# Kernel optimization log

Measured on AMD Instinct MI355X. Metric: run time of the kernel, lower is better.

The kernel has to match this reference:

```python
import jax, jax.numpy as jnp
import numpy as np

N, E, H, IN_NF, G, STEPS, EHID = 4096, 8192, 128, 64, 8, 3, 32


def setup_inputs() -> dict:
    key = jax.random.key(0)
    ks = jax.random.split(key, 24)

    def gn(k, shape, fan_in):
        return jax.random.normal(k, shape, dtype=jnp.float32) / np.sqrt(fan_in)

    inp = {
        "x": jax.random.normal(ks[0], (N, IN_NF), dtype=jnp.float32),
        "edge_index": jax.random.randint(ks[1], (2, E), 0, N, dtype=jnp.int32),
        "edge_attr": jax.random.uniform(ks[2], (E, 1), dtype=jnp.float32),
        "batch": jnp.sort(jax.random.randint(ks[3], (N,), 0, G, dtype=jnp.int32)),
        # lin0: in_nf -> hid
        "lin0_w": gn(ks[4], (IN_NF, H), IN_NF),
        "lin0_b": jnp.zeros((H,), jnp.float32),
        # per-step edge MLP: 1 -> 32 -> H*H (stacked over STEPS)
        "nn_w1": gn(ks[5], (STEPS, 1, EHID), 1),
        "nn_b1": jnp.zeros((STEPS, EHID), jnp.float32),
        "nn_w2": gn(ks[6], (STEPS, EHID, H * H), EHID) * 0.1,
        "nn_b2": jnp.zeros((STEPS, H * H), jnp.float32),
        # NNConv root weight (no bias) + conv bias, per step
        "root_w": gn(ks[7], (STEPS, H, H), H),
        "conv_b": jnp.zeros((STEPS, H), jnp.float32),
        # single-layer GRU (input H, hidden H); gate order r, z, n
        "gru_wih": gn(ks[8], (3 * H, H), H),
        "gru_whh": gn(ks[9], (3 * H, H), H),
        "gru_bih": jnp.zeros((3 * H,), jnp.float32),
        "gru_bhh": jnp.zeros((3 * H,), jnp.float32),
        # readout
        "lin1_w": gn(ks[10], (H, H // 2), H),
        "lin1_b": jnp.zeros((H // 2,), jnp.float32),
        "lin2_w": gn(ks[11], (H // 2, 1), H // 2),
        "lin2_b": jnp.zeros((1,), jnp.float32),
    }
    return inp


def _gru_cell(m, h, wih, whh, bih, bhh):
    gi = m @ wih.T + bih          # [N, 3H]
    gh = h @ whh.T + bhh          # [N, 3H]
    i_r, i_z, i_n = jnp.split(gi, 3, axis=-1)
    h_r, h_z, h_n = jnp.split(gh, 3, axis=-1)
    r = jax.nn.sigmoid(i_r + h_r)
    z = jax.nn.sigmoid(i_z + h_z)
    n = jnp.tanh(i_n + r * h_n)
    return (1.0 - z) * n + z * h


def reference(x, edge_index, edge_attr, batch, lin0_w, lin0_b, nn_w1, nn_b1,
              nn_w2, nn_b2, root_w, conv_b, gru_wih, gru_whh, gru_bih,
              gru_bhh, lin1_w, lin1_b, lin2_w, lin2_b):
    n_nodes = x.shape[0]
    row, col = edge_index[0], edge_index[1]  # source j -> target i

    x = jax.nn.relu(x @ lin0_w + lin0_b)     # [N, H]
    h = x

    # in-degree for mean aggregation (0-degree nodes -> 0 output)
    deg = jax.ops.segment_sum(jnp.ones((row.shape[0],), x.dtype), col,
                              num_segments=n_nodes)
    inv_deg = jnp.where(deg > 0, 1.0 / jnp.maximum(deg, 1.0), 0.0)[:, None]

    for t in range(STEPS):
        # edge-conditioned weights: [E, H, H]
        e_h = jax.nn.relu(edge_attr @ nn_w1[t] + nn_b1[t])
        w_e = (e_h @ nn_w2[t] + nn_b2[t]).reshape(-1, H, H)
        # gather -> per-edge matvec -> scatter-mean
        msg = jnp.einsum('eh,eho->eo', x[row], w_e)
        agg = jax.ops.segment_sum(msg, col, num_segments=n_nodes) * inv_deg
        m = jax.nn.relu(agg + x @ root_w[t] + conv_b[t])
        h = _gru_cell(m, h, gru_wih, gru_whh, gru_bih, gru_bhh)
        x = h

    # global mean pool over graphs
    cnt = jax.ops.segment_sum(jnp.ones((n_nodes,), x.dtype), batch,
                              num_segments=G)
    g = jax.ops.segment_sum(x, batch, num_segments=G) / jnp.maximum(cnt, 1.0)[:, None]
    g = jax.nn.relu(g @ lin1_w + lin1_b)  # dropout: eval mode (identity)
    out = g @ lin2_w + lin2_b             # [G, 1]
    return out
```

## Files before the change

### kernel.cpp

```cpp
#include <hip/hip_runtime.h>
#include <math.h>

#define NN 4096
#define EE 8192
#define HH 128
#define GG 8
#define MU 4096

typedef __attribute__((ext_vector_type(8))) _Float16 half8;
typedef __attribute__((ext_vector_type(4))) float floatx4;

__device__ __forceinline__ void ldst16(const _Float16* g, void* l) {
    __builtin_amdgcn_global_load_lds(
        (const __attribute__((address_space(1))) unsigned int*)g,
        (__attribute__((address_space(3))) unsigned int*)l, 16, 0, 0);
}

__device__ __forceinline__ unsigned f2u(float f) {
    unsigned b = __float_as_uint(f);
    return (b & 0x80000000u) ? ~b : (b | 0x80000000u);
}
__device__ __forceinline__ float u2f(unsigned u) {
    return __uint_as_float((u & 0x80000000u) ? (u ^ 0x80000000u) : ~u);
}

__device__ __forceinline__ int cls_k(float w, float b, float mn, float mx) {
    const float hi = w > 0.f ? w * mx + b : w * mn + b;
    const float lo = w > 0.f ? w * mn + b : w * mx + b;
    if (hi <= 0.f) return 0;
    if (lo >= 0.f) return 1;
    return 2;
}

__global__ __launch_bounds__(256) void ymix_k(
    const _Float16* __restrict__ A, const _Float16* __restrict__ BT3t,
    const float* __restrict__ w2t, _Float16* __restrict__ Y,
    _Float16* __restrict__ U, const int* __restrict__ kflag)
{
    __shared__ __align__(16) _Float16 As[128 * 32];
    __shared__ __align__(16) _Float16 Bs[128 * 32];
    const int tid = threadIdx.x;
    const int lane = tid & 63, wave = tid >> 6;
    const int m0 = blockIdx.y * 128;
    const int wr = (wave >> 1) * 64, wc = (wave & 1) * 64;
    const int fm = lane & 15, fq = lane >> 4;
    const int srow = tid >> 2, soff = (tid & 3) << 3;
    const _Float16* gA0 = A + (size_t)(m0 + srow) * 128 + soff;
    const _Float16* gA1 = gA0 + (size_t)64 * 128;
    char* lA0 = (char*)As + tid * 16;  char* lA1 = (char*)As + (tid + 256) * 16;
    char* lB0 = (char*)Bs + tid * 16;  char* lB1 = (char*)Bs + (tid + 256) * 16;
    const int bx = blockIdx.x;
    const int er = fq * 4, ec = fm;

    floatx4 acc[4][4] = {};
    if (bx < 3) {
        const _Float16* gB0 = BT3t + (size_t)(bx * 128 + srow) * 128 + soff;
        const _Float16* gB1 = gB0 + (size_t)64 * 128;
        for (int k0 = 0; k0 < 128; k0 += 32) {
            __syncthreads();
            ldst16(gA0 + k0, lA0); ldst16(gA1 + k0, lA1);
            ldst16(gB0 + k0, lB0); ldst16(gB1 + k0, lB1);
            __syncthreads();
            half8 af[4], bf[4];
#pragma unroll
            for (int i = 0; i < 4; ++i)
                af[i] = *(const half8*)&As[(wr + i * 16 + fm) * 32 + fq * 8];
#pragma unroll
            for (int j = 0; j < 4; ++j)
                bf[j] = *(const half8*)&Bs[(wc + j * 16 + fm) * 32 + fq * 8];
#pragma unroll
            for (int i = 0; i < 4; ++i)
#pragma unroll
                for (int j = 0; j < 4; ++j)
                    acc[i][j] = __builtin_amdgcn_mfma_f32_16x16x32_f16(
                        af[i], bf[j], acc[i][j], 0, 0, 0);
        }
#pragma unroll
        for (int i = 0; i < 4; ++i) {
            const int gr = m0 + wr + i * 16 + er;
#pragma unroll
            for (int j = 0; j < 4; ++j) {
                const int gc = bx * 128 + wc + j * 16 + ec;
#pragma unroll
                for (int r = 0; r < 4; ++r)
                    Y[(size_t)(gr + r) * 384 + gc] = (_Float16)acc[i][j][r];
            }
        }
    } else {
        const unsigned f = *(const unsigned*)kflag;
        const int kk = bx - 3;
        if (!((f >> kk) & 1u)) return;
        const int cbase = __popc(f & ((1u << kk) - 1u)) << 7;
        const float* w2s = w2t + (size_t)kk * 16384;
        for (int k0 = 0; k0 < 128; k0 += 32) {
            __syncthreads();
            ldst16(gA0 + k0, lA0); ldst16(gA1 + k0, lA1);
#pragma unroll
            for (int c = tid; c < 512; c += 256) {
                const int row = c >> 2, seg = (c & 3) << 3;
                _Float16 v8[8];
#pragma unroll
                for (int u = 0; u < 8; ++u)
                    v8[u] = (_Float16)w2s[(size_t)(k0 + seg + u) * 128 + row];
                *(half8*)&Bs[row * 32 + seg] = *(half8*)v8;
            }
            __syncthreads();
            half8 af[4], bf[4];
#pragma unroll
            for (int i = 0; i < 4; ++i)
                af[i] = *(const half8*)&As[(wr + i * 16 + fm) * 32 + fq * 8];
#pragma unroll
            for (int j = 0; j < 4; ++j)
                bf[j] = *(const half8*)&Bs[(wc + j * 16 + fm) * 32 + fq * 8];
#pragma unroll
            for (int i = 0; i < 4; ++i)
#pragma unroll
                for (int j = 0; j < 4; ++j)
                    acc[i][j] = __builtin_amdgcn_mfma_f32_16x16x32_f16(
                        af[i], bf[j], acc[i][j], 0, 0, 0);
        }
#pragma unroll
        for (int i = 0; i < 4; ++i) {
            const int gr = m0 + wr + i * 16 + er;
#pragma unroll
            for (int j = 0; j < 4; ++j) {
                const int gc = cbase + wc + j * 16 + ec;
#pragma unroll
                for (int r = 0; r < 4; ++r)
                    U[(size_t)(gr + r) * MU + gc] = (_Float16)acc[i][j][r];
            }
        }
    }
}

__global__ __launch_bounds__(256) void escat_k(
    const int2* __restrict__ rc, const float2* __restrict__ ec2,
    const float* __restrict__ ehPt, const _Float16* __restrict__ Y,
    const _Float16* __restrict__ U, float* __restrict__ mpre,
    const int* __restrict__ kflag)
{
    const int b = blockIdx.x;
    const int p0 = ((b & 7) * 512 + (b >> 3)) * 2;
    const int h2 = threadIdx.x >> 7;
    const int o = threadIdx.x & 127;
    const int p = p0 + h2;
    const int2 e = rc[p];
    const float2 c = ec2[p];
    const _Float16* Yr = Y + (size_t)e.x * 384;
    float acc = c.x * (float)Yr[o] + c.y * (float)Yr[128 + o];
    const unsigned f = *(const unsigned*)kflag;
    if (f) {
        const int nk = __popc(f);
        const _Float16* Ur = U + (size_t)e.x * MU;
        const float* ep = ehPt + (size_t)p * 32;
        for (int i = 0; i < nk; ++i)
            acc += ep[i] * (float)Ur[i * 128 + o];
    }
    atomicAdd(&mpre[(size_t)e.y * 128 + o], acc);
}

__global__ __launch_bounds__(256) void gru_k(
    const float* __restrict__ mpre, const _Float16* __restrict__ Y,
    const float* __restrict__ cb, const _Float16* __restrict__ Ax,
    const _Float16* __restrict__ Bih, const _Float16* __restrict__ Bhh,
    const float* __restrict__ bih, const float* __restrict__ bhh,
    float* __restrict__ g1, float* __restrict__ g2)
{
    const int z = blockIdx.z;
    const _Float16* B = z ? Bhh : Bih;
    const float* bias = z ? bhh : bih;
    float* C = z ? g2 : g1;

    __shared__ __align__(16) _Float16 As[128 * 40];
    __shared__ __align__(16) _Float16 Bs[128 * 40];
    const int tid = threadIdx.x;
    const int lane = tid & 63, wave = tid >> 6;
    const int m0 = blockIdx.y * 128, n0 = blockIdx.x * 128;
    const int wr = (wave >> 1) * 64, wc = (wave & 1) * 64;
    const int fm = lane & 15, fq = lane >> 4;

    floatx4 acc[4][4] = {};
    for (int k0 = 0; k0 < 128; k0 += 32) {
        __syncthreads();
#pragma unroll
        for (int c = tid; c < 512; c += 256) {
            const int row = c >> 2, seg = (c & 3) << 3;
            if (z == 0) {
                const int mr = m0 + row;
                const half8 yv = *(const half8*)&Y[(size_t)mr * 384 + 256 + k0 + seg];
                const float4 a0 = *(const float4*)&mpre[(size_t)mr * 128 + k0 + seg];
                const float4 a1 = *(const float4*)&mpre[(size_t)mr * 128 + k0 + seg + 4];
                const float4 c0 = *(const float4*)&cb[k0 + seg];
                const float4 c1 = *(const float4*)&cb[k0 + seg + 4];
                _Float16 v8[8];
                float v;
                v = (float)yv[0] + a0.x + c0.x; v8[0] = (_Float16)(v > 0.f ? v : 0.f);
                v = (float)yv[1] + a0.y + c0.y; v8[1] = (_Float16)(v > 0.f ? v : 0.f);
                v = (float)yv[2] + a0.z + c0.z; v8[2] = (_Float16)(v > 0.f ? v : 0.f);
                v = (float)yv[3] + a0.w + c0.w; v8[3] = (_Float16)(v > 0.f ? v : 0.f);
                v = (float)yv[4] + a1.x + c1.x; v8[4] = (_Float16)(v > 0.f ? v : 0.f);
                v = (float)yv[5] + a1.y + c1.y; v8[5] = (_Float16)(v > 0.f ? v : 0.f);
                v = (float)yv[6] + a1.z + c1.z; v8[6] = (_Float16)(v > 0.f ? v : 0.f);
                v = (float)yv[7] + a1.w + c1.w; v8[7] = (_Float16)(v > 0.f ? v : 0.f);
                *(half8*)&As[row * 40 + seg] = *(half8*)v8;
            } else {
                *(half8*)&As[row * 40 + seg] =
                    *(const half8*)&Ax[(size_t)(m0 + row) * 128 + k0 + seg];
            }
            *(half8*)&Bs[row * 40 + seg] =
                *(const half8*)&B[(size_t)(n0 + row) * 128 + k0 + seg];
        }
        __syncthreads();
        half8 af[4], bf[4];
#pragma unroll
        for (int i = 0; i < 4; ++i)
            af[i] = *(const half8*)&As[(wr + i * 16 + fm) * 40 + fq * 8];
#pragma unroll
        for (int j = 0; j < 4; ++j)
            bf[j] = *(const half8*)&Bs[(wc + j * 16 + fm) * 40 + fq * 8];
#pragma unroll
        for (int i = 0; i < 4; ++i)
#pragma unroll
            for (int j = 0; j < 4; ++j)
                acc[i][j] = __builtin_amdgcn_mfma_f32_16x16x32_f16(
                    af[i], bf[j], acc[i][j], 0, 0, 0);
    }
    const int er = fq * 4, ec = fm;
#pragma unroll
    for (int i = 0; i < 4; ++i) {
        const int gr = m0 + wr + i * 16 + er;
#pragma unroll
        for (int j = 0; j < 4; ++j) {
            const int gc = n0 + wc + j * 16 + ec;
            const float bv = bias[gc];
#pragma unroll
            for (int r = 0; r < 4; ++r)
                C[(size_t)(gr + r) * 384 + gc] = acc[i][j][r] + bv;
        }
    }
}

__global__ void gate_k(const float* __restrict__ G1, const float* __restrict__ G2,
                       float* __restrict__ xh, _Float16* __restrict__ Ax,
                       const int* __restrict__ batch, float* __restrict__ pooled) {
    const int idx = blockIdx.x * 256 + threadIdx.x;
    const int n = idx >> 7, o = idx & 127;
    const size_t b = (size_t)n * 384;
    float ir = G1[b + o], iz = G1[b + 128 + o], in_ = G1[b + 256 + o];
    float hr = G2[b + o], hz = G2[b + 128 + o], hn = G2[b + 256 + o];
    float r = 1.f / (1.f + expf(-(ir + hr)));
    float z = 1.f / (1.f + expf(-(iz + hz)));
    float nv = tanhf(in_ + r * hn);
    float hv = (1.f - z) * nv + z * xh[idx];
    xh[idx] = hv;
    Ax[idx] = (_Float16)hv;
    if (pooled) atomicAdd(&pooled[batch[n] * 128 + o], hv);
}

__global__ __launch_bounds__(256) void setup_lin0_k(
    const float* __restrict__ wih, const float* __restrict__ whh,
    _Float16* __restrict__ Bih, _Float16* __restrict__ Bhh,
    const int* __restrict__ ei, const float* __restrict__ eattr,
    const int* __restrict__ batch,
    float* __restrict__ deg, int* __restrict__ odeg, float* __restrict__ cnt,
    unsigned* __restrict__ eaMM,
    const float* __restrict__ x, const float* __restrict__ l0w,
    const float* __restrict__ l0b, float* __restrict__ xh,
    _Float16* __restrict__ Ax)
{
    __shared__ float loc8[GG];
    __shared__ float As[16][64];
    __shared__ float Bs[16][64];
    const int b = blockIdx.x, t = threadIdx.x;
    if (b < 192) {
        const int idx = b * 256 + t;
        Bih[idx] = (_Float16)wih[idx];
        Bhh[idx] = (_Float16)whh[idx];
    } else if (b < 224) {
        const int e = (b - 192) * 256 + t;
        atomicAdd(&deg[ei[EE + e]], 1.0f);
        atomicAdd(&odeg[ei[e]], 1);
        const float ea = eattr[e];
        unsigned u1 = f2u(ea), u2 = f2u(-ea);
#pragma unroll
        for (int off = 32; off > 0; off >>= 1) {
            unsigned o1 = __shfl_down(u1, off), o2 = __shfl_down(u2, off);
            u1 = u1 > o1 ? u1 : o1;  u2 = u2 > o2 ? u2 : o2;
        }
        if ((t & 63) == 0) { atomicMax(&eaMM[0], u1); atomicMax(&eaMM[1], u2); }
    } else if (b < 240) {
        const int n = (b - 224) * 256 + t;
        if (t < GG) loc8[t] = 0.f;
        __syncthreads();
        atomicAdd(&loc8[batch[n]], 1.0f);
        __syncthreads();
        if (t < GG) atomicAdd(&cnt[t], loc8[t]);
    } else {
        const int bb = b - 240;
        const int j0 = (bb & 1) * 64;
        const int m0 = (bb >> 1) * 64;
        const int tx = t & 15, ty = t >> 4;
        const int arow = t >> 2, acol = (t & 3) << 2;
        const int bk = t >> 4, bj = (t & 15) << 2;
        float c[4][4] = {};
        for (int k0 = 0; k0 < 64; k0 += 16) {
            __syncthreads();
            float4 av = *(const float4*)&x[(size_t)(m0 + arow) * 64 + k0 + acol];
            As[acol + 0][arow] = av.x;
            As[acol + 1][arow] = av.y;
            As[acol + 2][arow] = av.z;
            As[acol + 3][arow] = av.w;
            *(float4*)&Bs[bk][bj] = *(const float4*)&l0w[(size_t)(k0 + bk) * 128 + j0 + bj];
            __syncthreads();
#pragma unroll
            for (int kk = 0; kk < 16; ++kk) {
                const float4 a = *(const float4*)&As[kk][ty << 2];
                const float4 bv = *(const float4*)&Bs[kk][tx << 2];
                c[0][0] += a.x * bv.x; c[0][1] += a.x * bv.y; c[0][2] += a.x * bv.z; c[0][3] += a.x * bv.w;
                c[1][0] += a.y * bv.x; c[1][1] += a.y * bv.y; c[1][2] += a.y * bv.z; c[1][3] += a.y * bv.w;
                c[2][0] += a.z * bv.x; c[2][1] += a.z * bv.y; c[2][2] += a.z * bv.z; c[2][3] += a.z * bv.w;
                c[3][0] += a.w * bv.x; c[3][1] += a.w * bv.y; c[3][2] += a.w * bv.z; c[3][3] += a.w * bv.w;
            }
        }
        const float4 bv = *(const float4*)&l0b[j0 + (tx << 2)];
        const int col0 = j0 + (tx << 2);
#pragma unroll
        for (int i = 0; i < 4; ++i) {
            const int row = m0 + (ty << 2) + i;
            float4 o;
            o.x = fmaxf(c[i][0] + bv.x, 0.f); o.y = fmaxf(c[i][1] + bv.y, 0.f);
            o.z = fmaxf(c[i][2] + bv.z, 0.f); o.w = fmaxf(c[i][3] + bv.w, 0.f);
            *(float4*)&xh[(size_t)row * 128 + col0] = o;
            _Float16* base = Ax + (size_t)row * 128 + col0;
            base[0] = (_Float16)o.x; base[1] = (_Float16)o.y;
            base[2] = (_Float16)o.z; base[3] = (_Float16)o.w;
        }
    }
}

__global__ __launch_bounds__(256) void scan_wsum_k(
    const int* __restrict__ odeg, int* __restrict__ ocur,
    const float* __restrict__ w1, const float* __restrict__ b1,
    const float* __restrict__ w2, const float* __restrict__ b2,
    const float* __restrict__ rw, const unsigned* __restrict__ eaMM,
    _Float16* __restrict__ BT3)
{
    const int t = threadIdx.x;
    if (blockIdx.x == 0) {
        __shared__ int ps[256];
        const int base = t * 16;
        int l[16]; int s = 0;
#pragma unroll
        for (int i = 0; i < 16; ++i) { l[i] = s; s += odeg[base + i]; }
        ps[t] = s;
        __syncthreads();
        for (int d = 1; d < 256; d <<= 1) {
            int v = (t >= d) ? ps[t - d] : 0;
            __syncthreads();
            ps[t] += v;
            __syncthreads();
        }
        const int excl = (t == 0) ? 0 : ps[t - 1];
#pragma unroll
        for (int i = 0; i < 16; ++i) ocur[base + i] = excl + l[i];
    } else {
        __shared__ float wl[32], bl[32];
        const int bb = blockIdx.x - 1;
        const int st = bb >> 6;
        if (t < 32) {
            const float w = w1[st * 32 + t], bv = b1[st * 32 + t];
            const float mx = u2f(eaMM[0]), mn = -u2f(eaMM[1]);
            const int c = cls_k(w, bv, mn, mx);
            wl[t] = (c == 1) ? w : 0.f;
            bl[t] = (c == 1) ? bv : 0.f;
        }
        __syncthreads();
        const int idx = (bb & 63) * 256 + t;
        const int h = idx >> 7, o = idx & 127;
        const float* W2t = w2 + (size_t)st * 524288;
        float a = 0.f, c2 = 0.f;
#pragma unroll 8
        for (int j = 0; j < 32; ++j) {
            const float v = W2t[(size_t)j * 16384 + idx];
            a += wl[j] * v; c2 += bl[j] * v;
        }
        c2 += b2[(size_t)st * 16384 + idx];
        _Float16* B = BT3 + (size_t)st * 49152;
        B[(size_t)o * 128 + h]         = (_Float16)a;
        B[(size_t)(128 + o) * 128 + h] = (_Float16)c2;
        B[(size_t)(256 + o) * 128 + h] = (_Float16)rw[(size_t)st * 16384 + idx];
    }
}

__global__ __launch_bounds__(256) void scatter_k(
    const int* __restrict__ ei, const float* __restrict__ eattr,
    const float* __restrict__ w1, const float* __restrict__ b1,
    const float* __restrict__ deg, int* __restrict__ ocur,
    const unsigned* __restrict__ eaMM,
    int2* __restrict__ rc, float2* __restrict__ ec2,
    float* __restrict__ ehP, int* __restrict__ kflag)
{
    __shared__ unsigned mm[3];
    if (threadIdx.x < 3) mm[threadIdx.x] = 0u;
    __syncthreads();
    if (threadIdx.x < 96) {
        const int tt = threadIdx.x >> 5, k = threadIdx.x & 31;
        const float w = w1[tt * 32 + k], bv = b1[tt * 32 + k];
        const float mx = u2f(eaMM[0]), mn = -u2f(eaMM[1]);
        if (cls_k(w, bv, mn, mx) == 2) atomicOr(&mm[tt], 1u << k);
    }
    __syncthreads();
    const int wave = threadIdx.x >> 6, lane = threadIdx.x & 63;
    const int e = blockIdx.x * 4 + wave;
    const int r = ei[e], c = ei[EE + e];
    int pos = 0;
    if (lane == 0) pos = atomicAdd(&ocur[r], 1);
    pos = __shfl(pos, 0);
    const float d = deg[c];
    const float inv = d > 0.f ? 1.0f / d : 0.0f;
    const float ea = eattr[e];
    if (lane == 0) {
        rc[pos] = make_int2(r, c);
        ec2[pos] = make_float2(ea * inv, inv);
    }
#pragma unroll
    for (int t = 0; t < 3; ++t) {
        const unsigned m = mm[t];
        if (lane < 32 && ((m >> lane) & 1u)) {
            const float v = ea * w1[t * 32 + lane] + b1[t * 32 + lane];
            const int slot = __popc(m & ((1u << lane) - 1u));
            ehP[((size_t)t * EE + pos) * 32 + slot] = (v > 0.f ? v : 0.f) * inv;
        }
    }
    if (threadIdx.x < 3) kflag[threadIdx.x] = (int)mm[threadIdx.x];
}

__global__ __launch_bounds__(128) void final_k(
    const float* __restrict__ pooled, const float* __restrict__ cnt,
    const float* __restrict__ l1w, const float* __restrict__ l1b,
    const float* __restrict__ l2w, const float* __restrict__ l2b,
    float* __restrict__ out)
{
    __shared__ float gv[128];
    const int g = blockIdx.x, t = threadIdx.x;
    float c = cnt[g]; c = c > 1.f ? c : 1.f;
    gv[t] = pooled[g * 128 + t] / c;
    __syncthreads();
    if (t < 64) {
        float y = l1b[t];
        for (int h = 0; h < 128; ++h) y += gv[h] * l1w[h * 64 + t];
        y = y > 0.f ? y : 0.f;
        float s = y * l2w[t];
#pragma unroll
        for (int off = 32; off > 0; off >>= 1)
            s += __shfl_down(s, off);
        if (t == 0) out[g] = s + l2b[0];
    }
}

extern "C" void kernel_launch(void* const* d_in, const int* in_sizes, int n_in,
                              void* d_out, int out_size, void* d_ws, size_t ws_size,
                              hipStream_t stream) {
    const float* x      = (const float*)d_in[0];
    const int*   ei     = (const int*)d_in[1];
    const float* eattr  = (const float*)d_in[2];
    const int*   batch  = (const int*)d_in[3];
    const float* lin0_w = (const float*)d_in[4];
    const float* lin0_b = (const float*)d_in[5];
    const float* nn_w1  = (const float*)d_in[6];
    const float* nn_b1  = (const float*)d_in[7];
    const float* nn_w2  = (const float*)d_in[8];
    const float* nn_b2  = (const float*)d_in[9];
    const float* root_w = (const float*)d_in[10];
    const float* conv_b = (const float*)d_in[11];
    const float* gwih   = (const float*)d_in[12];
    const float* gwhh   = (const float*)d_in[13];
    const float* gbih   = (const float*)d_in[14];
    const float* gbhh   = (const float*)d_in[15];
    const float* l1w    = (const float*)d_in[16];
    const float* l1b    = (const float*)d_in[17];
    const float* l2w    = (const float*)d_in[18];
    const float* l2b    = (const float*)d_in[19];
    float* out = (float*)d_out;
    float* ws  = (float*)d_ws;

    float*    mpre0  = ws;
    float*    pooled = ws + 1572864;
    float*    cnt    = ws + 1573888;
    float*    deg    = ws + 1573896;
    int*      odeg   = (int*)(ws + 1577992);
    unsigned* eaMM   = (unsigned*)(ws + 1582088);
    int*      kflag  = (int*)(ws + 1582090);
    int*      ocur   = (int*)(ws + 1582096);
    int2*     rc     = (int2*)(ws + 1586192);
    float2*   ec2    = (float2*)(ws + 1602576);
    float*    ehP    = ws + 1618960;
    float*    xh     = ws + 2405392;
    float*    g1     = ws + 2929680;
    float*    g2     = ws + 4502544;
    _Float16* Y      = (_Float16*)(ws + 6075408);
    _Float16* U      = (_Float16*)(ws + 6861840);
    _Float16* Ax     = (_Float16*)(ws + 15250448);
    _Float16* BT3    = (_Float16*)(ws + 15512592);
    _Float16* Bih16  = (_Float16*)(ws + 15586320);
    _Float16* Bhh16  = (_Float16*)(ws + 15610896);

    hipMemsetAsync(mpre0, 0, 6328384, stream);
    setup_lin0_k<<<368, 256, 0, stream>>>(gwih, gwhh, Bih16, Bhh16, ei, eattr,
                                          batch, deg, odeg, cnt, eaMM,
                                          x, lin0_w, lin0_b, xh, Ax);
    scan_wsum_k<<<193, 256, 0, stream>>>(odeg, ocur, nn_w1, nn_b1, nn_w2,
                                         nn_b2, root_w, eaMM, BT3);
    scatter_k<<<2048, 256, 0, stream>>>(ei, eattr, nn_w1, nn_b1, deg, ocur,
                                        eaMM, rc, ec2, ehP, kflag);

    for (int t = 0; t < 3; ++t) {
        float* mpre = mpre0 + (size_t)t * 524288;
        ymix_k<<<dim3(35, 32), 256, 0, stream>>>(
            Ax, BT3 + (size_t)t * 49152, nn_w2 + (size_t)t * 524288, Y, U, kflag + t);
        escat_k<<<4096, 256, 0, stream>>>(rc, ec2, ehP + (size_t)t * EE * 32,
                                          Y, U, mpre, kflag + t);
        gru_k<<<dim3(3, 32, 2), 256, 0, stream>>>(mpre, Y, conv_b + t * 128, Ax,
                                                  Bih16, Bhh16, gbih, gbhh, g1, g2);
        gate_k<<<2048, 256, 0, stream>>>(g1, g2, xh, Ax, batch,
                                         (t == 2) ? pooled : nullptr);
    }

    final_k<<<GG, 128, 0, stream>>>(pooled, cnt, l1w, l1b, l2w, l2b, out);
}
```

Before: 216.4 us.

## Fuse edge scatter into GRU input GEMM via CSR by destination, move gh into ymix

Edges are now sorted by destination node, with a row pointer built in the scan, so each GRU tile block can accumulate its 128 nodes' messages into shared memory with LDS atomics. This removes the separate escat kernel, the global atomics and the global mpre buffer along with its memset. The hidden-state GEMM (h·Whh) moves into the ymix kernel as three extra column blocks, which cuts one launch per step. In exchange, each of the 3 column blocks recomputes the per-edge messages for its node tile (threefold redundant gather work), only 96 blocks run the fused kernel, and a large LDS array lowers occupancy.

```diff
diff --git a/kernel.cpp b/kernel.cpp
--- a/kernel.cpp
+++ b/kernel.cpp
@@ -6,6 +6,7 @@
 #define HH 128
 #define GG 8
 #define MU 4096
+#define MMW 129
 
 typedef __attribute__((ext_vector_type(8))) _Float16 half8;
 typedef __attribute__((ext_vector_type(4))) float floatx4;
@@ -32,10 +33,12 @@
     return 2;
 }
 
-__global__ __launch_bounds__(256) void ymix_k(
+__global__ __launch_bounds__(256) void ymix_gh_k(
     const _Float16* __restrict__ A, const _Float16* __restrict__ BT3t,
+    const _Float16* __restrict__ Bhh, const float* __restrict__ bhh,
     const float* __restrict__ w2t, _Float16* __restrict__ Y,
-    _Float16* __restrict__ U, const int* __restrict__ kflag)
+    float* __restrict__ g2, _Float16* __restrict__ U,
+    const int* __restrict__ kflag)
 {
     __shared__ __align__(16) _Float16 As[128 * 32];
     __shared__ __align__(16) _Float16 Bs[128 * 32];
@@ -53,8 +56,10 @@
     const int er = fq * 4, ec = fm;
 
     floatx4 acc[4][4] = {};
-    if (bx < 3) {
-        const _Float16* gB0 = BT3t + (size_t)(bx * 128 + srow) * 128 + soff;
+    if (bx < 6) {
+        const _Float16* gB0 = (bx < 3)
+            ? BT3t + (size_t)(bx * 128 + srow) * 128 + soff
+            : Bhh + (size_t)((bx - 3) * 128 + srow) * 128 + soff;
         const _Float16* gB1 = gB0 + (size_t)64 * 128;
         for (int k0 = 0; k0 < 128; k0 += 32) {
             __syncthreads();
@@ -75,20 +80,36 @@
                     acc[i][j] = __builtin_amdgcn_mfma_f32_16x16x32_f16(
                         af[i], bf[j], acc[i][j], 0, 0, 0);
         }
-#pragma unroll
-        for (int i = 0; i < 4; ++i) {
-            const int gr = m0 + wr + i * 16 + er;
-#pragma unroll
-            for (int j = 0; j < 4; ++j) {
-                const int gc = bx * 128 + wc + j * 16 + ec;
-#pragma unroll
-                for (int r = 0; r < 4; ++r)
-                    Y[(size_t)(gr + r) * 384 + gc] = (_Float16)acc[i][j][r];
+        if (bx < 3) {
+#pragma unroll
+            for (int i = 0; i < 4; ++i) {
+                const int gr = m0 + wr + i * 16 + er;
+#pragma unroll
+                for (int j = 0; j < 4; ++j) {
+                    const int gc = bx * 128 + wc + j * 16 + ec;
+#pragma unroll
+                    for (int r = 0; r < 4; ++r)
+                        Y[(size_t)(gr + r) * 384 + gc] = (_Float16)acc[i][j][r];
+                }
+            }
+        } else {
+            const int n0 = (bx - 3) * 128;
+#pragma unroll
+            for (int i = 0; i < 4; ++i) {
+                const int gr = m0 + wr + i * 16 + er;
+#pragma unroll
+                for (int j = 0; j < 4; ++j) {
+                    const int gc = n0 + wc + j * 16 + ec;
+                    const float bv = bhh[gc];
+#pragma unroll
+                    for (int r = 0; r < 4; ++r)
+                        g2[(size_t)(gr + r) * 384 + gc] = acc[i][j][r] + bv;
+                }
             }
         }
     } else {
         const unsigned f = *(const unsigned*)kflag;
-        const int kk = bx - 3;
+        const int kk = bx - 6;
         if (!((f >> kk) & 1u)) return;
         const int cbase = __popc(f & ((1u << kk) - 1u)) << 7;
         const float* w2s = w2t + (size_t)kk * 16384;
@@ -133,82 +154,70 @@
     }
 }
 
-__global__ __launch_bounds__(256) void escat_k(
+__global__ __launch_bounds__(256) void gruz0_k(
     const int2* __restrict__ rc, const float2* __restrict__ ec2,
     const float* __restrict__ ehPt, const _Float16* __restrict__ Y,
-    const _Float16* __restrict__ U, float* __restrict__ mpre,
+    const _Float16* __restrict__ U, const float* __restrict__ cb,
+    const _Float16* __restrict__ Bih, const float* __restrict__ bih,
+    const int* __restrict__ rowptr, float* __restrict__ g1,
     const int* __restrict__ kflag)
 {
-    const int b = blockIdx.x;
-    const int p0 = ((b & 7) * 512 + (b >> 3)) * 2;
-    const int h2 = threadIdx.x >> 7;
-    const int o = threadIdx.x & 127;
-    const int p = p0 + h2;
-    const int2 e = rc[p];
-    const float2 c = ec2[p];
-    const _Float16* Yr = Y + (size_t)e.x * 384;
-    float acc = c.x * (float)Yr[o] + c.y * (float)Yr[128 + o];
-    const unsigned f = *(const unsigned*)kflag;
-    if (f) {
-        const int nk = __popc(f);
-        const _Float16* Ur = U + (size_t)e.x * MU;
-        const float* ep = ehPt + (size_t)p * 32;
-        for (int i = 0; i < nk; ++i)
-            acc += ep[i] * (float)Ur[i * 128 + o];
-    }
-    atomicAdd(&mpre[(size_t)e.y * 128 + o], acc);
-}
-
-__global__ __launch_bounds__(256) void gru_k(
-    const float* __restrict__ mpre, const _Float16* __restrict__ Y,
-    const float* __restrict__ cb, const _Float16* __restrict__ Ax,
-    const _Float16* __restrict__ Bih, const _Float16* __restrict__ Bhh,
-    const float* __restrict__ bih, const float* __restrict__ bhh,
-    float* __restrict__ g1, float* __restrict__ g2)
-{
-    const int z = blockIdx.z;
-    const _Float16* B = z ? Bhh : Bih;
-    const float* bias = z ? bhh : bih;
-    float* C = z ? g2 : g1;
-
+    __shared__ float mm[128 * MMW];
     __shared__ __align__(16) _Float16 As[128 * 40];
     __shared__ __align__(16) _Float16 Bs[128 * 40];
     const int tid = threadIdx.x;
     const int lane = tid & 63, wave = tid >> 6;
-    const int m0 = blockIdx.y * 128, n0 = blockIdx.x * 128;
+    const int n0 = blockIdx.x * 128, m0 = blockIdx.y * 128;
     const int wr = (wave >> 1) * 64, wc = (wave & 1) * 64;
     const int fm = lane & 15, fq = lane >> 4;
 
+#pragma unroll
+    for (int i = tid; i < 128 * MMW; i += 256) mm[i] = 0.f;
+    __syncthreads();
+
+    const int start = rowptr[m0];
+    const int end = (m0 + 128 < NN) ? rowptr[m0 + 128] : EE;
+    const int h2 = tid >> 7, o = tid & 127;
+    const unsigned f = *(const unsigned*)kflag;
+    const int nk = __popc(f);
+    for (int p = start + h2; p < end; p += 2) {
+        const int2 e = rc[p];
+        const float2 c = ec2[p];
+        const _Float16* Yr = Y + (size_t)e.x * 384;
+        float v = c.x * (float)Yr[o] + c.y * (float)Yr[128 + o];
+        if (f) {
+            const _Float16* Ur = U + (size_t)e.x * MU;
+            const float* ep = ehPt + (size_t)p * 32;
+            for (int i = 0; i < nk; ++i)
+                v += ep[i] * (float)Ur[i * 128 + o];
+        }
+        atomicAdd(&mm[(e.y - m0) * MMW + o], v);
+    }
+    __syncthreads();
+
     floatx4 acc[4][4] = {};
     for (int k0 = 0; k0 < 128; k0 += 32) {
-        __syncthreads();
 #pragma unroll
         for (int c = tid; c < 512; c += 256) {
             const int row = c >> 2, seg = (c & 3) << 3;
-            if (z == 0) {
-                const int mr = m0 + row;
-                const half8 yv = *(const half8*)&Y[(size_t)mr * 384 + 256 + k0 + seg];
-                const float4 a0 = *(const float4*)&mpre[(size_t)mr * 128 + k0 + seg];
-                const float4 a1 = *(const float4*)&mpre[(size_t)mr * 128 + k0 + seg + 4];
-                const float4 c0 = *(const float4*)&cb[k0 + seg];
-                const float4 c1 = *(const float4*)&cb[k0 + seg + 4];
-                _Float16 v8[8];
-                float v;
-                v = (float)yv[0] + a0.x + c0.x; v8[0] = (_Float16)(v > 0.f ? v : 0.f);
-                v = (float)yv[1] + a0.y + c0.y; v8[1] = (_Float16)(v > 0.f ? v : 0.f);
-                v = (float)yv[2] + a0.z + c0.z; v8[2] = (_Float16)(v > 0.f ? v : 0.f);
-                v = (float)yv[3] + a0.w + c0.w; v8[3] = (_Float16)(v > 0.f ? v : 0.f);
-                v = (float)yv[4] + a1.x + c1.x; v8[4] = (_Float16)(v > 0.f ? v : 0.f);
-                v = (float)yv[5] + a1.y + c1.y; v8[5] = (_Float16)(v > 0.f ? v : 0.f);
-                v = (float)yv[6] + a1.z + c1.z; v8[6] = (_Float16)(v > 0.f ? v : 0.f);
-                v = (float)yv[7] + a1.w + c1.w; v8[7] = (_Float16)(v > 0.f ? v : 0.f);
-                *(half8*)&As[row * 40 + seg] = *(half8*)v8;
-            } else {
-                *(half8*)&As[row * 40 + seg] =
-                    *(const half8*)&Ax[(size_t)(m0 + row) * 128 + k0 + seg];
-            }
+            const int mr = m0 + row;
+            const half8 yv = *(const half8*)&Y[(size_t)mr * 384 + 256 + k0 + seg];
+            const float4 c0 = *(const float4*)&cb[k0 + seg];
+            const float4 c1 = *(const float4*)&cb[k0 + seg + 4];
+            const float* mrow = &mm[row * MMW + k0 + seg];
+            _Float16 v8[8];
+            float v;
+            v = (float)yv[0] + mrow[0] + c0.x; v8[0] = (_Float16)(v > 0.f ? v : 0.f);
+            v = (float)yv[1] + mrow[1] + c0.y; v8[1] = (_Float16)(v > 0.f ? v : 0.f);
+            v = (float)yv[2] + mrow[2] + c0.z; v8[2] = (_Float16)(v > 0.f ? v : 0.f);
+            v = (float)yv[3] + mrow[3] + c0.w; v8[3] = (_Float16)(v > 0.f ? v : 0.f);
+            v = (float)yv[4] + mrow[4] + c1.x; v8[4] = (_Float16)(v > 0.f ? v : 0.f);
+            v = (float)yv[5] + mrow[5] + c1.y; v8[5] = (_Float16)(v > 0.f ? v : 0.f);
+            v = (float)yv[6] + mrow[6] + c1.z; v8[6] = (_Float16)(v > 0.f ? v : 0.f);
+            v = (float)yv[7] + mrow[7] + c1.w; v8[7] = (_Float16)(v > 0.f ? v : 0.f);
+            *(half8*)&As[row * 40 + seg] = *(half8*)v8;
             *(half8*)&Bs[row * 40 + seg] =
-                *(const half8*)&B[(size_t)(n0 + row) * 128 + k0 + seg];
+                *(const half8*)&Bih[(size_t)(n0 + row) * 128 + k0 + seg];
         }
         __syncthreads();
         half8 af[4], bf[4];
@@ -224,6 +233,7 @@
             for (int j = 0; j < 4; ++j)
                 acc[i][j] = __builtin_amdgcn_mfma_f32_16x16x32_f16(
                     af[i], bf[j], acc[i][j], 0, 0, 0);
+        __syncthreads();
     }
     const int er = fq * 4, ec = fm;
 #pragma unroll
@@ -232,10 +242,10 @@
 #pragma unroll
         for (int j = 0; j < 4; ++j) {
             const int gc = n0 + wc + j * 16 + ec;
-            const float bv = bias[gc];
+            const float bv = bih[gc];
 #pragma unroll
             for (int r = 0; r < 4; ++r)
-                C[(size_t)(gr + r) * 384 + gc] = acc[i][j][r] + bv;
+                g1[(size_t)(gr + r) * 384 + gc] = acc[i][j][r] + bv;
         }
     }
 }
@@ -262,7 +272,7 @@
     _Float16* __restrict__ Bih, _Float16* __restrict__ Bhh,
     const int* __restrict__ ei, const float* __restrict__ eattr,
     const int* __restrict__ batch,
-    float* __restrict__ deg, int* __restrict__ odeg, float* __restrict__ cnt,
+    float* __restrict__ deg, int* __restrict__ ideg, float* __restrict__ cnt,
     unsigned* __restrict__ eaMM,
     const float* __restrict__ x, const float* __restrict__ l0w,
     const float* __restrict__ l0b, float* __restrict__ xh,
@@ -278,8 +288,9 @@
         Bhh[idx] = (_Float16)whh[idx];
     } else if (b < 224) {
         const int e = (b - 192) * 256 + t;
-        atomicAdd(&deg[ei[EE + e]], 1.0f);
-        atomicAdd(&odeg[ei[e]], 1);
+        const int c = ei[EE + e];
+        atomicAdd(&deg[c], 1.0f);
+        atomicAdd(&ideg[c], 1);
         const float ea = eattr[e];
         unsigned u1 = f2u(ea), u2 = f2u(-ea);
 #pragma unroll
@@ -339,7 +350,8 @@
 }
 
 __global__ __launch_bounds__(256) void scan_wsum_k(
-    const int* __restrict__ odeg, int* __restrict__ ocur,
+    const int* __restrict__ ideg, int* __restrict__ ocur,
+    int* __restrict__ rowptr,
     const float* __restrict__ w1, const float* __restrict__ b1,
     const float* __restrict__ w2, const float* __restrict__ b2,
     const float* __restrict__ rw, const unsigned* __restrict__ eaMM,
@@ -351,7 +363,7 @@
         const int base = t * 16;
         int l[16]; int s = 0;
 #pragma unroll
-        for (int i = 0; i < 16; ++i) { l[i] = s; s += odeg[base + i]; }
+        for (int i = 0; i < 16; ++i) { l[i] = s; s += ideg[base + i]; }
         ps[t] = s;
         __syncthreads();
         for (int d = 1; d < 256; d <<= 1) {
@@ -362,7 +374,11 @@
         }
         const int excl = (t == 0) ? 0 : ps[t - 1];
 #pragma unroll
-        for (int i = 0; i < 16; ++i) ocur[base + i] = excl + l[i];
+        for (int i = 0; i < 16; ++i) {
+            const int v = excl + l[i];
+            ocur[base + i] = v;
+            rowptr[base + i] = v;
+        }
     } else {
         __shared__ float wl[32], bl[32];
         const int bb = blockIdx.x - 1;
@@ -414,7 +430,7 @@
     const int e = blockIdx.x * 4 + wave;
     const int r = ei[e], c = ei[EE + e];
     int pos = 0;
-    if (lane == 0) pos = atomicAdd(&ocur[r], 1);
+    if (lane == 0) pos = atomicAdd(&ocur[c], 1);
     pos = __shfl(pos, 0);
     const float d = deg[c];
     const float inv = d > 0.f ? 1.0f / d : 0.0f;
@@ -484,44 +500,43 @@
     float* out = (float*)d_out;
     float* ws  = (float*)d_ws;
 
-    float*    mpre0  = ws;
-    float*    pooled = ws + 1572864;
-    float*    cnt    = ws + 1573888;
-    float*    deg    = ws + 1573896;
-    int*      odeg   = (int*)(ws + 1577992);
-    unsigned* eaMM   = (unsigned*)(ws + 1582088);
-    int*      kflag  = (int*)(ws + 1582090);
-    int*      ocur   = (int*)(ws + 1582096);
-    int2*     rc     = (int2*)(ws + 1586192);
-    float2*   ec2    = (float2*)(ws + 1602576);
-    float*    ehP    = ws + 1618960;
-    float*    xh     = ws + 2405392;
-    float*    g1     = ws + 2929680;
-    float*    g2     = ws + 4502544;
-    _Float16* Y      = (_Float16*)(ws + 6075408);
-    _Float16* U      = (_Float16*)(ws + 6861840);
-    _Float16* Ax     = (_Float16*)(ws + 15250448);
-    _Float16* BT3    = (_Float16*)(ws + 15512592);
-    _Float16* Bih16  = (_Float16*)(ws + 15586320);
-    _Float16* Bhh16  = (_Float16*)(ws + 15610896);
-
-    hipMemsetAsync(mpre0, 0, 6328384, stream);
+    float*    pooled = ws;
+    float*    cnt    = ws + 1024;
+    float*    deg    = ws + 1032;
+    int*      ideg   = (int*)(ws + 5128);
+    unsigned* eaMM   = (unsigned*)(ws + 9224);
+    int*      kflag  = (int*)(ws + 9226);
+    int*      ocur   = (int*)(ws + 9232);
+    int*      rowptr = (int*)(ws + 13328);
+    int2*     rc     = (int2*)(ws + 17424);
+    float2*   ec2    = (float2*)(ws + 33808);
+    float*    ehP    = ws + 50192;
+    float*    xh     = ws + 836624;
+    float*    g1     = ws + 1360912;
+    float*    g2     = ws + 2933776;
+    _Float16* Y      = (_Float16*)(ws + 4506640);
+    _Float16* Ax     = (_Float16*)(ws + 5293072);
+    _Float16* BT3    = (_Float16*)(ws + 5555216);
+    _Float16* Bih16  = (_Float16*)(ws + 5628944);
+    _Float16* Bhh16  = (_Float16*)(ws + 5653520);
+    _Float16* U      = (_Float16*)(ws + 5678096);
+
+    hipMemsetAsync(pooled, 0, 36928, stream);
     setup_lin0_k<<<368, 256, 0, stream>>>(gwih, gwhh, Bih16, Bhh16, ei, eattr,
-                                          batch, deg, odeg, cnt, eaMM,
+                                          batch, deg, ideg, cnt, eaMM,
                                           x, lin0_w, lin0_b, xh, Ax);
-    scan_wsum_k<<<193, 256, 0, stream>>>(odeg, ocur, nn_w1, nn_b1, nn_w2,
-                                         nn_b2, root_w, eaMM, BT3);
+    scan_wsum_k<<<193, 256, 0, stream>>>(ideg, ocur, rowptr, nn_w1, nn_b1,
+                                         nn_w2, nn_b2, root_w, eaMM, BT3);
     scatter_k<<<2048, 256, 0, stream>>>(ei, eattr, nn_w1, nn_b1, deg, ocur,
                                         eaMM, rc, ec2, ehP, kflag);
 
     for (int t = 0; t < 3; ++t) {
-        float* mpre = mpre0 + (size_t)t * 524288;
-        ymix_k<<<dim3(35, 32), 256, 0, stream>>>(
-            Ax, BT3 + (size_t)t * 49152, nn_w2 + (size_t)t * 524288, Y, U, kflag + t);
-        escat_k<<<4096, 256, 0, stream>>>(rc, ec2, ehP + (size_t)t * EE * 32,
-                                          Y, U, mpre, kflag + t);
-        gru_k<<<dim3(3, 32, 2), 256, 0, stream>>>(mpre, Y, conv_b + t * 128, Ax,
-                                                  Bih16, Bhh16, gbih, gbhh, g1, g2);
+        ymix_gh_k<<<dim3(38, 32), 256, 0, stream>>>(
+            Ax, BT3 + (size_t)t * 49152, Bhh16, gbhh,
+            nn_w2 + (size_t)t * 524288, Y, g2, U, kflag + t);
+        gruz0_k<<<dim3(3, 32), 256, 0, stream>>>(
+            rc, ec2, ehP + (size_t)t * EE * 32, Y, U, conv_b + t * 128,
+            Bih16, gbih, rowptr, g1, kflag + t);
         gate_k<<<2048, 256, 0, stream>>>(g1, g2, xh, Ax, batch,
                                          (t == 2) ? pooled : nullptr);
     }
```

New measurement: 397.7 us. 83.8% more time.
